# Kernel tuning notes

Measured on AMD Instinct MI355X. Metric: run time of the kernel, lower is better.

Reference implementation:

```python
import jax, jax.numpy as jnp
import numpy as np

N = 50000      # total nodes
C = 128        # in_channels
G = 4          # num_groups
B = 50         # number of graphs
NPG = N // B   # nodes per graph = 1000
E = 250000     # total edges (intra-graph)
COUT = 128     # conv out_channels


def setup_inputs() -> dict:
    key = jax.random.key(0)
    ks = jax.random.split(key, 6)
    sc = 1.0 / np.sqrt(C)
    x = jax.random.normal(ks[0], (N, C), dtype=jnp.float32)
    W_group = jax.random.normal(ks[1], (C, G), dtype=jnp.float32) * sc
    W_self = jax.random.normal(ks[2], (C, COUT), dtype=jnp.float32) * sc
    W_nbr = jax.random.normal(ks[3], (C, COUT), dtype=jnp.float32) * sc
    b = jnp.zeros((COUT,), dtype=jnp.float32)
    # intra-graph edges: E//B edges per graph, endpoints offset by graph id
    epg = E // B
    offs = (jnp.arange(E, dtype=jnp.int32) // epg) * NPG
    src = offs + jax.random.randint(ks[4], (E,), 0, NPG, dtype=jnp.int32)
    dst = offs + jax.random.randint(ks[5], (E,), 0, NPG, dtype=jnp.int32)
    edge_index = jnp.stack([src, dst])
    batch = (jnp.arange(N, dtype=jnp.int32) // NPG)
    # expanded node e = i*G*NPG + g*NPG + j maps back to original node i*NPG + j
    eidx = jnp.arange(G * N, dtype=jnp.int32)
    group_ptr = (eidx // (G * NPG)) * NPG + (eidx % NPG)
    return dict(x=x, W_group=W_group, W_self=W_self, W_nbr=W_nbr, b=b,
                edge_index=edge_index, batch=batch, group_ptr=group_ptr)


def reference(x, W_group, W_self, W_nbr, b, edge_index, batch, group_ptr):
    # soft group assignment: s = softmax(x @ W_group).T -> [G, N]
    s = jax.nn.softmax(x @ W_group, axis=-1).T
    # outer-product expansion: [G, N, C]
    ex = s[:, :, None] * x[None, :, :]
    # per-graph cat ordering: (g, graph i, local j) -> i*G*NPG + g*NPG + j
    ex = ex.reshape(G, B, NPG, C).transpose(1, 0, 2, 3).reshape(G * N, C)
    # expanded adjacency: replicate each graph's edges once per group
    src, dst = edge_index[0], edge_index[1]
    goff = jnp.arange(G, dtype=src.dtype)[:, None] * NPG            # [G, 1]
    src_exp = ((src // NPG) * (G * NPG))[None, :] + goff + (src % NPG)[None, :]
    dst_exp = ((dst // NPG) * (G * NPG))[None, :] + goff + (dst % NPG)[None, :]
    src_exp = src_exp.reshape(-1)
    dst_exp = dst_exp.reshape(-1)
    # GraphConv on expanded graph: self transform + sum-aggregated neighbor transform
    msg = (ex @ W_nbr)[src_exp]                                      # [G*E, COUT]
    agg = jax.ops.segment_sum(msg, dst_exp, num_segments=G * N)
    out = ex @ W_self + agg + b                                      # [G*N, COUT]
    # scatter-reduce G group copies back onto N original nodes
    return jax.ops.segment_sum(out, group_ptr, num_segments=N)
```

## Files before the change

kernel.cpp:

```cpp
#include <hip/hip_runtime.h>

constexpr int N_NODES  = 50000;
constexpr int C_IN     = 128;
constexpr int C_OUT    = 128;
constexpr int E_EDGES  = 250000;
constexpr int G_GRP    = 4;
constexpr int NPG      = 1000;
constexpr int TM       = 32;
constexpr int CAP      = 32;
constexpr int NXCD     = 8;


typedef __attribute__((ext_vector_type(8))) short     short8;
typedef __attribute__((ext_vector_type(4))) float     f32x4;
typedef __attribute__((ext_vector_type(2))) unsigned  u32x2;

__device__ __forceinline__ unsigned short f2bf(float f) {
    unsigned u = __builtin_bit_cast(unsigned, f);
    u += 0x7fffu + ((u >> 16) & 1u);
    return (unsigned short)(u >> 16);
}
__device__ __forceinline__ unsigned pack2(float lo, float hi) {
    return (unsigned)f2bf(lo) | ((unsigned)f2bf(hi) << 16);
}

constexpr int EDGE_BLOCKS = (E_EDGES + 255) / 256;
constexpr int WPREP_BLOCKS = (C_OUT * 256) / 256;

__global__ __launch_bounds__(256) void fill_prep_kernel(
    const int* __restrict__ src, const int* __restrict__ dst,
    int* __restrict__ cnt, int* __restrict__ buckets,
    const float* __restrict__ Wself, const float* __restrict__ Wnbr,
    unsigned short* __restrict__ WT)
{
    int b = blockIdx.x;
    if (b < EDGE_BLOCKS) {
        int e = b * 256 + threadIdx.x;
        if (e < E_EDGES) {
            int d = dst[e];
            int pos = atomicAdd(&cnt[d], 1);
            if (pos < CAP) buckets[(size_t)d * CAP + pos] = src[e];
        }
    } else {
        int idx = (b - EDGE_BLOCKS) * 256 + threadIdx.x;
        int c = idx >> 8, k = idx & 255;
        float v = (k < 128) ? Wself[k * C_OUT + c] : Wnbr[(k - 128) * C_OUT + c];
        WT[idx] = f2bf(v);
    }
}

constexpr int FUSED_BLOCKS = (N_NODES + TM - 1) / TM;

__global__ __launch_bounds__(256) void fused_gather_mfma(
    const float* __restrict__ x,
    const int* __restrict__ cnt,
    const int* __restrict__ buckets,
    const unsigned short* __restrict__ WT,
    const float* __restrict__ bias,
    float* __restrict__ out)
{
    __shared__ unsigned char Ab[TM * 512];

    int wg;
    {
        constexpr int q = FUSED_BLOCKS / NXCD;
        constexpr int r = FUSED_BLOCKS % NXCD;
        int xcd = blockIdx.x % NXCD;
        int lid = blockIdx.x / NXCD;
        wg = (xcd < r ? xcd * (q + 1) : r * (q + 1) + (xcd - r) * q) + lid;
    }

    const int tid  = threadIdx.x;
    const int row0 = wg * TM;

    #pragma unroll
    for (int i = 0; i < 4; ++i) {
        int idx = tid + i * 256;
        int r = idx >> 5, q = idx & 31;
        int n = row0 + r;
        float4 v = make_float4(0.f, 0.f, 0.f, 0.f);
        if (n < N_NODES) v = reinterpret_cast<const float4*>(x)[(size_t)n * 32 + q];
        unsigned lo = pack2(v.x, v.y), hi = pack2(v.z, v.w);
        int byte = (r * 512 + q * 8) ^ ((r & 7) << 4);
        *reinterpret_cast<u32x2*>(&Ab[byte]) = u32x2{lo, hi};
    }

    {
        const int grp = tid >> 5;
        const int q   = tid & 31;
        const float4* x4 = reinterpret_cast<const float4*>(x);
        #pragma unroll
        for (int h = 0; h < 4; ++h) {
            int r = grp + h * 8;
            int n = row0 + r;
            float ax = 0.f, ay = 0.f, az = 0.f, aw = 0.f;
            if (n < N_NODES) {
                int d = cnt[n];
                if (d > CAP) d = CAP;
                const int* sp = buckets + (size_t)n * CAP;
                int e = 0;
                for (; e + 4 <= d; e += 4) {
                    int s0 = sp[e], s1 = sp[e + 1], s2 = sp[e + 2], s3 = sp[e + 3];
                    float4 v0 = x4[(size_t)s0 * 32 + q];
                    float4 v1 = x4[(size_t)s1 * 32 + q];
                    float4 v2 = x4[(size_t)s2 * 32 + q];
                    float4 v3 = x4[(size_t)s3 * 32 + q];
                    ax += (v0.x + v1.x) + (v2.x + v3.x);
                    ay += (v0.y + v1.y) + (v2.y + v3.y);
                    az += (v0.z + v1.z) + (v2.z + v3.z);
                    aw += (v0.w + v1.w) + (v2.w + v3.w);
                }
                for (; e < d; ++e) {
                    int s = sp[e];
                    float4 v = x4[(size_t)s * 32 + q];
                    ax += v.x; ay += v.y; az += v.z; aw += v.w;
                }
            }
            unsigned lo = pack2(ax, ay), hi = pack2(az, aw);
            int byte = (r * 512 + 256 + q * 8) ^ ((r & 7) << 4);
            *reinterpret_cast<u32x2*>(&Ab[byte]) = u32x2{lo, hi};
        }
    }
    __syncthreads();

    const int lane = tid & 63;
    const int w    = tid >> 6;
    const int rt   = w >> 1;
    const int ct0  = (w & 1) * 4;

    short8 a[8];
    {
        int r  = rt * 16 + (lane & 15);
        int kb = (lane >> 4) * 16;
        #pragma unroll
        for (int ks = 0; ks < 8; ++ks) {
            int byte = (r * 512 + ks * 64 + kb) ^ ((r & 7) << 4);
            a[ks] = *reinterpret_cast<const short8*>(&Ab[byte]);
        }
    }

    #pragma unroll
    for (int cti = 0; cti < 4; ++cti) {
        int ct = ct0 + cti;
        int c  = ct * 16 + (lane & 15);
        const short8* bp = reinterpret_cast<const short8*>(WT + (size_t)c * 256)
                           + (lane >> 4);
        f32x4 acc = {0.f, 0.f, 0.f, 0.f};
        #pragma unroll
        for (int ks = 0; ks < 8; ++ks) {
            short8 b = bp[ks * 4];
            acc = __builtin_amdgcn_mfma_f32_16x16x32_bf16(a[ks], b, acc, 0, 0, 0);
        }
        float bv = (float)G_GRP * bias[c];
        #pragma unroll
        for (int i = 0; i < 4; ++i) {
            int rr = row0 + rt * 16 + (lane >> 4) * 4 + i;
            if (rr < N_NODES) out[(size_t)rr * C_OUT + c] = acc[i] + bv;
        }
    }
}

extern "C" void kernel_launch(void* const* d_in, const int* in_sizes, int n_in,
                              void* d_out, int out_size, void* d_ws, size_t ws_size,
                              hipStream_t stream)
{
    const float* x     = (const float*)d_in[0];
    const float* Wself = (const float*)d_in[2];
    const float* Wnbr  = (const float*)d_in[3];
    const float* bias  = (const float*)d_in[4];
    const int*   eidx  = (const int*)d_in[5];

    const int* src = eidx;
    const int* dst = eidx + E_EDGES;

    int* cnt     = (int*)d_ws;
    int* buckets = cnt + N_NODES;
    unsigned short* WT = (unsigned short*)(buckets + (size_t)N_NODES * CAP);

    float* out = (float*)d_out;

    hipMemsetAsync(cnt, 0, (size_t)N_NODES * sizeof(int), stream);

    fill_prep_kernel<<<EDGE_BLOCKS + WPREP_BLOCKS, 256, 0, stream>>>(
        src, dst, cnt, buckets, Wself, Wnbr, WT);

    fused_gather_mfma<<<FUSED_BLOCKS, 256, 0, stream>>>(
        x, cnt, buckets, WT, bias, out);
}
```

Before: 63.42 us.

## Split neighbor gather into separate kernel writing bf16 aggregates

Splits the fused gather+MFMA kernel into two kernels. A standalone gather kernel uses 8 nodes per 256-thread block to sum neighbor features and writes them to a bf16 workspace buffer. The GEMM kernel then just loads these aggregates into shared memory. The aim is more parallelism and better latency hiding for the irregular gather, in exchange for an extra launch and a round-trip of the aggregate through global memory.

```diff
diff --git a/kernel.cpp b/kernel.cpp
--- a/kernel.cpp
+++ b/kernel.cpp
@@ -5,7 +5,6 @@
 constexpr int C_OUT    = 128;
 constexpr int E_EDGES  = 250000;
 constexpr int G_GRP    = 4;
-constexpr int NPG      = 1000;
 constexpr int TM       = 32;
 constexpr int CAP      = 32;
 constexpr int NXCD     = 8;
@@ -24,7 +23,13 @@
     return (unsigned)f2bf(lo) | ((unsigned)f2bf(hi) << 16);
 }
 
-constexpr int EDGE_BLOCKS = (E_EDGES + 255) / 256;
+__device__ __forceinline__ int xcd_swizzle(int bid, int nblocks) {
+    int q = nblocks / NXCD, r = nblocks % NXCD;
+    int xcd = bid % NXCD, lid = bid / NXCD;
+    return (xcd < r ? xcd * (q + 1) : r * (q + 1) + (xcd - r) * q) + lid;
+}
+
+constexpr int EDGE_BLOCKS  = (E_EDGES + 255) / 256;
 constexpr int WPREP_BLOCKS = (C_OUT * 256) / 256;
 
 __global__ __launch_bounds__(256) void fill_prep_kernel(
@@ -49,27 +54,59 @@
     }
 }
 
-constexpr int FUSED_BLOCKS = (N_NODES + TM - 1) / TM;
-
-__global__ __launch_bounds__(256) void fused_gather_mfma(
+constexpr int GATHER_BLOCKS = N_NODES / 8;
+
+__global__ __launch_bounds__(256) void gather_kernel(
     const float* __restrict__ x,
     const int* __restrict__ cnt,
     const int* __restrict__ buckets,
+    unsigned short* __restrict__ xa_bf)
+{
+    int wg   = xcd_swizzle(blockIdx.x, GATHER_BLOCKS);
+    int tid  = threadIdx.x;
+    int n    = wg * 8 + (tid >> 5);
+    int q    = tid & 31;
+
+    const float4* x4 = reinterpret_cast<const float4*>(x);
+    int d = cnt[n];
+    if (d > CAP) d = CAP;
+    const int* sp = buckets + (size_t)n * CAP;
+
+    float ax = 0.f, ay = 0.f, az = 0.f, aw = 0.f;
+    int e = 0;
+    for (; e + 4 <= d; e += 4) {
+        int s0 = sp[e], s1 = sp[e + 1], s2 = sp[e + 2], s3 = sp[e + 3];
+        float4 v0 = x4[(size_t)s0 * 32 + q];
+        float4 v1 = x4[(size_t)s1 * 32 + q];
+        float4 v2 = x4[(size_t)s2 * 32 + q];
+        float4 v3 = x4[(size_t)s3 * 32 + q];
+        ax += (v0.x + v1.x) + (v2.x + v3.x);
+        ay += (v0.y + v1.y) + (v2.y + v3.y);
+        az += (v0.z + v1.z) + (v2.z + v3.z);
+        aw += (v0.w + v1.w) + (v2.w + v3.w);
+    }
+    for (; e < d; ++e) {
+        int s = sp[e];
+        float4 v = x4[(size_t)s * 32 + q];
+        ax += v.x; ay += v.y; az += v.z; aw += v.w;
+    }
+
+    u32x2 pk{pack2(ax, ay), pack2(az, aw)};
+    *reinterpret_cast<u32x2*>(&xa_bf[(size_t)n * 128 + q * 4]) = pk;
+}
+
+constexpr int GEMM_BLOCKS = (N_NODES + TM - 1) / TM;
+
+__global__ __launch_bounds__(256) void mfma_gemm_kernel(
+    const float* __restrict__ x,
+    const unsigned short* __restrict__ xa_bf,
     const unsigned short* __restrict__ WT,
     const float* __restrict__ bias,
     float* __restrict__ out)
 {
     __shared__ unsigned char Ab[TM * 512];
 
-    int wg;
-    {
-        constexpr int q = FUSED_BLOCKS / NXCD;
-        constexpr int r = FUSED_BLOCKS % NXCD;
-        int xcd = blockIdx.x % NXCD;
-        int lid = blockIdx.x / NXCD;
-        wg = (xcd < r ? xcd * (q + 1) : r * (q + 1) + (xcd - r) * q) + lid;
-    }
-
+    int wg = xcd_swizzle(blockIdx.x, GEMM_BLOCKS);
     const int tid  = threadIdx.x;
     const int row0 = wg * TM;
 
@@ -85,41 +122,16 @@
         *reinterpret_cast<u32x2*>(&Ab[byte]) = u32x2{lo, hi};
     }
 
-    {
-        const int grp = tid >> 5;
-        const int q   = tid & 31;
-        const float4* x4 = reinterpret_cast<const float4*>(x);
-        #pragma unroll
-        for (int h = 0; h < 4; ++h) {
-            int r = grp + h * 8;
-            int n = row0 + r;
-            float ax = 0.f, ay = 0.f, az = 0.f, aw = 0.f;
-            if (n < N_NODES) {
-                int d = cnt[n];
-                if (d > CAP) d = CAP;
-                const int* sp = buckets + (size_t)n * CAP;
-                int e = 0;
-                for (; e + 4 <= d; e += 4) {
-                    int s0 = sp[e], s1 = sp[e + 1], s2 = sp[e + 2], s3 = sp[e + 3];
-                    float4 v0 = x4[(size_t)s0 * 32 + q];
-                    float4 v1 = x4[(size_t)s1 * 32 + q];
-                    float4 v2 = x4[(size_t)s2 * 32 + q];
-                    float4 v3 = x4[(size_t)s3 * 32 + q];
-                    ax += (v0.x + v1.x) + (v2.x + v3.x);
-                    ay += (v0.y + v1.y) + (v2.y + v3.y);
-                    az += (v0.z + v1.z) + (v2.z + v3.z);
-                    aw += (v0.w + v1.w) + (v2.w + v3.w);
-                }
-                for (; e < d; ++e) {
-                    int s = sp[e];
-                    float4 v = x4[(size_t)s * 32 + q];
-                    ax += v.x; ay += v.y; az += v.z; aw += v.w;
-                }
-            }
-            unsigned lo = pack2(ax, ay), hi = pack2(az, aw);
-            int byte = (r * 512 + 256 + q * 8) ^ ((r & 7) << 4);
-            *reinterpret_cast<u32x2*>(&Ab[byte]) = u32x2{lo, hi};
-        }
+    #pragma unroll
+    for (int i = 0; i < 4; ++i) {
+        int idx = tid + i * 256;
+        int r = idx >> 5, q = idx & 31;
+        int n = row0 + r;
+        u32x2 pk{0u, 0u};
+        if (n < N_NODES)
+            pk = *reinterpret_cast<const u32x2*>(&xa_bf[(size_t)n * 128 + q * 4]);
+        int byte = (r * 512 + 256 + q * 8) ^ ((r & 7) << 4);
+        *reinterpret_cast<u32x2*>(&Ab[byte]) = pk;
     }
     __syncthreads();
 
@@ -175,7 +187,8 @@
 
     int* cnt     = (int*)d_ws;
     int* buckets = cnt + N_NODES;
-    unsigned short* WT = (unsigned short*)(buckets + (size_t)N_NODES * CAP);
+    unsigned short* WT    = (unsigned short*)(buckets + (size_t)N_NODES * CAP);
+    unsigned short* xa_bf = WT + (size_t)C_OUT * 256;
 
     float* out = (float*)d_out;
 
@@ -184,6 +197,8 @@
     fill_prep_kernel<<<EDGE_BLOCKS + WPREP_BLOCKS, 256, 0, stream>>>(
         src, dst, cnt, buckets, Wself, Wnbr, WT);
 
-    fused_gather_mfma<<<FUSED_BLOCKS, 256, 0, stream>>>(
-        x, cnt, buckets, WT, bias, out);
-}
+    gather_kernel<<<GATHER_BLOCKS, 256, 0, stream>>>(x, cnt, buckets, xa_bf);
+
+    mfma_gemm_kernel<<<GEMM_BLOCKS, 256, 0, stream>>>(
+        x, xa_bf, WT, bias, out);
+}
```

Result: slower. 67.38 us (+6.3%).
